# Kernel optimization log

Hardware: AMD Instinct MI355X
Metric: run time of the kernel (lower is better)

## Reference

```python
import jax, jax.numpy as jnp
import numpy as np

N_NODES = 100000
N_EDGES = 1600000
N_GRAPHS = 256
IN_C = 64
HID = 128
OUT = 128
BN_EPS = 1e-5


def setup_inputs() -> dict:
    key = jax.random.key(0)
    ks = jax.random.split(key, 24)
    x = jax.random.normal(ks[0], (N_NODES, IN_C), jnp.float32)
    edge_index = jax.random.randint(ks[1], (2, N_EDGES), 0, N_NODES, dtype=jnp.int64 if jax.config.jax_enable_x64 else jnp.int32)
    batch = jnp.sort(jax.random.randint(ks[2], (N_NODES,), 0, N_GRAPHS))

    def lin(k, i, o):
        return (jax.random.normal(k, (i, o), jnp.float32) / np.float32(np.sqrt(i)))

    d = {"x": x, "edge_index": edge_index, "batch": batch}
    in_dims = [IN_C, HID, HID]
    for l in range(3):
        d[f"w1_{l}"] = lin(ks[3 + 6 * l], in_dims[l], HID)
        d[f"b1_{l}"] = jnp.zeros((HID,), jnp.float32)
        d[f"w2_{l}"] = lin(ks[4 + 6 * l], HID, HID)
        d[f"b2_{l}"] = jnp.zeros((HID,), jnp.float32)
        d[f"gamma_{l}"] = jnp.ones((HID,), jnp.float32)
        d[f"beta_{l}"] = jnp.zeros((HID,), jnp.float32)
    d["proj_w"] = lin(ks[22], HID, OUT)
    d["proj_b"] = jnp.zeros((OUT,), jnp.float32)
    return d


def _gin_forward(x, edge_index, batch, layers, proj_w, proj_b):
    src, dst = edge_index[0], edge_index[1]
    h = x
    for (w1, b1, w2, b2, g, b) in layers:
        # GINConv (eps=0, aggr='add'): MLP(h_i + sum_{j->i} h_j)
        agg = jax.ops.segment_sum(h[src], dst, num_segments=h.shape[0])
        z = h + agg
        z = jax.nn.relu(z @ w1 + b1) @ w2 + b2
        # BatchNorm1d, training mode (biased batch stats)
        mean = z.mean(axis=0)
        var = z.var(axis=0)
        z = (z - mean) * jax.lax.rsqrt(var + BN_EPS) * g + b
        h = jax.nn.relu(z)
    # global_mean_pool over graph ids
    s = jax.ops.segment_sum(h, batch, num_segments=N_GRAPHS)
    cnt = jax.ops.segment_sum(jnp.ones((h.shape[0], 1), h.dtype), batch, num_segments=N_GRAPHS)
    hg = s / jnp.maximum(cnt, 1.0)
    return hg @ proj_w + proj_b


def reference(x, edge_index, batch,
              w1_0, b1_0, w2_0, b2_0, gamma_0, beta_0,
              w1_1, b1_1, w2_1, b2_1, gamma_1, beta_1,
              w1_2, b1_2, w2_2, b2_2, gamma_2, beta_2,
              proj_w, proj_b):
    layers = [
        (w1_0, b1_0, w2_0, b2_0, gamma_0, beta_0),
        (w1_1, b1_1, w2_1, b2_1, gamma_1, beta_1),
        (w1_2, b1_2, w2_2, b2_2, gamma_2, beta_2),
    ]
    return _gin_forward(x, edge_index, batch, layers, proj_w, proj_b)
```

## Files before the change

### kernel.cpp

```cpp
#include <hip/hip_runtime.h>

#define N_NODES 100000
#define N_EDGES 1600000
#define N_GRAPHS 256
#define HID 128
#define BN_EPS 1e-5f

#define NT 1563
#define EB 4096
#define RB 391
#define MB 1563

typedef __bf16 bf16x8 __attribute__((ext_vector_type(8)));
typedef __bf16 bf16x4 __attribute__((ext_vector_type(4)));
typedef __bf16 bf16x2 __attribute__((ext_vector_type(2)));
typedef float f32x4 __attribute__((ext_vector_type(4)));

__global__ __launch_bounds__(256) void prep_all_kernel(
    const float* __restrict__ wa, const float* __restrict__ wb,
    const float* __restrict__ wc, const float* __restrict__ wd,
    const float* __restrict__ we, const float* __restrict__ wf,
    __bf16* __restrict__ wt) {
  int idx = blockIdx.x * 256 + threadIdx.x;
  if (idx >= 90112) return;
  const float* w;
  int K, local;
  if (idx < 8192) { w = wa; K = 64; local = idx; }
  else {
    int s = (idx - 8192) / 16384;
    local = (idx - 8192) - s * 16384;
    K = 128;
    w = (s == 0) ? wb : (s == 1) ? wc : (s == 2) ? wd : (s == 3) ? we : wf;
  }
  int n = local / K, k = local - n * K;
  wt[idx] = (__bf16)w[k * 128 + n];
}

__global__ __launch_bounds__(256) void x_convert_kernel(const float* __restrict__ x,
                                                        __bf16* __restrict__ xb) {
  int idx = blockIdx.x * 256 + threadIdx.x;
  if (idx >= N_NODES * 16) return;
  f32x4 v = ((const f32x4*)x)[idx];
  bf16x4 o = {(__bf16)v[0], (__bf16)v[1], (__bf16)v[2], (__bf16)v[3]};
  ((bf16x4*)xb)[idx] = o;
}

__global__ __launch_bounds__(256) void tile_hist_kernel(const int* __restrict__ ei,
                                                        int* __restrict__ tcnt) {
  __shared__ int hist[NT];
  int t = threadIdx.x;
  for (int i = t; i < NT; i += 256) hist[i] = 0;
  __syncthreads();
  int base = blockIdx.x * EB;
#pragma unroll 4
  for (int i = 0; i < EB / 256; i++) {
    int e = base + i * 256 + t;
    if (e < N_EDGES) atomicAdd(&hist[ei[N_EDGES + e] >> 6], 1);
  }
  __syncthreads();
  for (int i = t; i < NT; i += 256) {
    int h = hist[i];
    if (h) atomicAdd(&tcnt[i], h);
  }
}

__global__ __launch_bounds__(256) void tile_scan_kernel(const int* __restrict__ tcnt,
                                                        int* __restrict__ tstart,
                                                        int* __restrict__ gcursor) {
  __shared__ int ps[256];
  int t = threadIdx.x;
  const int CH = (NT + 255) / 256;
  int lo = t * CH, hi = min(lo + CH, NT);
  int s = 0;
  for (int i = lo; i < hi; i++) s += tcnt[i];
  ps[t] = s;
  __syncthreads();
  for (int off = 1; off < 256; off <<= 1) {
    int v = ps[t];
    int u = (t >= off) ? ps[t - off] : 0;
    __syncthreads();
    ps[t] = v + u;
    __syncthreads();
  }
  int base = (t == 0) ? 0 : ps[t - 1];
  for (int i = lo; i < hi; i++) {
    tstart[i] = base;
    gcursor[i] = base;
    base += tcnt[i];
  }
  if (t == 0) tstart[NT] = N_EDGES;
}

__global__ __launch_bounds__(256) void reorder2_kernel(const int* __restrict__ ei,
                                                       int* __restrict__ gcursor,
                                                       int* __restrict__ epack) {
  __shared__ int hist[NT];
  int t = threadIdx.x;
  for (int i = t; i < NT; i += 256) hist[i] = 0;
  __syncthreads();
  int base = blockIdx.x * EB;
#pragma unroll 4
  for (int i = 0; i < EB / 256; i++) {
    int e = base + i * 256 + t;
    if (e < N_EDGES) atomicAdd(&hist[ei[N_EDGES + e] >> 6], 1);
  }
  __syncthreads();
  for (int i = t; i < NT; i += 256) {
    int h = hist[i];
    if (h) hist[i] = atomicAdd(&gcursor[i], h);
  }
  __syncthreads();
#pragma unroll 4
  for (int i = 0; i < EB / 256; i++) {
    int e = base + i * 256 + t;
    if (e < N_EDGES) {
      int d = ei[N_EDGES + e];
      int s = ei[e];
      int pos = atomicAdd(&hist[d >> 6], 1);
      epack[pos] = (s << 6) | (d & 63);
    }
  }
}

__global__ __launch_bounds__(256) void row_sort_kernel(const int* __restrict__ tstart,
                                                       const int* __restrict__ epack,
                                                       int* __restrict__ starts,
                                                       int* __restrict__ srcs) {
  __shared__ int cnt[64];
  __shared__ int rbase[65];
  __shared__ int rofs[64];
  int t = threadIdx.x, b = blockIdx.x;
  int ts = tstart[b], te = tstart[b + 1];
  if (t < 64) cnt[t] = 0;
  __syncthreads();
  for (int i = ts + t; i < te; i += 256) atomicAdd(&cnt[epack[i] & 63], 1);
  __syncthreads();
  if (t == 0) {
    int a = 0;
    for (int r = 0; r < 64; r++) { rbase[r] = a; a += cnt[r]; }
    rbase[64] = a;
  }
  __syncthreads();
  if (t < 64) rofs[t] = ts + rbase[t];
  if (t <= 64) {
    int gr = b * 64 + t;
    if (gr <= N_NODES) starts[gr] = ts + rbase[t];
  }
  __syncthreads();
  for (int i = ts + t; i < te; i += 256) {
    int p = epack[i];
    int pos = atomicAdd(&rofs[p & 63], 1);
    srcs[pos] = p >> 6;
  }
}

__global__ __launch_bounds__(256) void h_apply_kernel(const __bf16* __restrict__ u,
                                                      const float* __restrict__ bnab,
                                                      __bf16* __restrict__ h) {
  int idx = blockIdx.x * 256 + threadIdx.x;
  if (idx >= N_NODES * (HID / 8)) return;
  int c8 = idx & 15;
  bf16x8 v = ((const bf16x8*)u)[idx];
  f32x4 a0 = ((const f32x4*)bnab)[c8 * 2];
  f32x4 a1 = ((const f32x4*)bnab)[c8 * 2 + 1];
  f32x4 b0 = ((const f32x4*)(bnab + HID))[c8 * 2];
  f32x4 b1 = ((const f32x4*)(bnab + HID))[c8 * 2 + 1];
  bf16x8 o;
#pragma unroll
  for (int k = 0; k < 4; k++) {
    o[k] = (__bf16)fmaxf(fmaf(a0[k], (float)v[k], b0[k]), 0.f);
    o[4 + k] = (__bf16)fmaxf(fmaf(a1[k], (float)v[4 + k], b1[k]), 0.f);
  }
  ((bf16x8*)h)[idx] = o;
}

template <int C>
__global__ __launch_bounds__(256) void gather_kernel(const __bf16* __restrict__ h,
                                                     const int* __restrict__ starts,
                                                     const int* __restrict__ srcs,
                                                     __bf16* __restrict__ z) {
  const int lane = threadIdx.x & 63;
  const int row = blockIdx.x * 4 + (threadIdx.x >> 6);
  if (row >= N_NODES) return;
  int e0 = starts[row], e1 = starts[row + 1];
  int deg = e1 - e0;
  int idxv = srcs[min(e0 + lane, N_EDGES - 1)];
  int dcap = min(deg, 64);
  if constexpr (C == 64) {
    float acc = (float)h[(size_t)row * 64 + lane];
    float s0 = 0.f, s1 = 0.f, s2 = 0.f, s3 = 0.f, s4 = 0.f, s5 = 0.f, s6 = 0.f, s7 = 0.f;
    int j = 0;
    for (; j + 7 < dcap; j += 8) {
      int i0 = __builtin_amdgcn_readlane(idxv, j);
      int i1 = __builtin_amdgcn_readlane(idxv, j + 1);
      int i2 = __builtin_amdgcn_readlane(idxv, j + 2);
      int i3 = __builtin_amdgcn_readlane(idxv, j + 3);
      int i4 = __builtin_amdgcn_readlane(idxv, j + 4);
      int i5 = __builtin_amdgcn_readlane(idxv, j + 5);
      int i6 = __builtin_amdgcn_readlane(idxv, j + 6);
      int i7 = __builtin_amdgcn_readlane(idxv, j + 7);
      float v0 = (float)h[(size_t)i0 * 64 + lane];
      float v1 = (float)h[(size_t)i1 * 64 + lane];
      float v2 = (float)h[(size_t)i2 * 64 + lane];
      float v3 = (float)h[(size_t)i3 * 64 + lane];
      float v4 = (float)h[(size_t)i4 * 64 + lane];
      float v5 = (float)h[(size_t)i5 * 64 + lane];
      float v6 = (float)h[(size_t)i6 * 64 + lane];
      float v7 = (float)h[(size_t)i7 * 64 + lane];
      s0 += v0; s1 += v1; s2 += v2; s3 += v3;
      s4 += v4; s5 += v5; s6 += v6; s7 += v7;
    }
    for (; j < dcap; j++) {
      int i0 = __builtin_amdgcn_readlane(idxv, j);
      s0 += (float)h[(size_t)i0 * 64 + lane];
    }
    for (int e = e0 + 64; e < e1; e++) s0 += (float)h[(size_t)srcs[e] * 64 + lane];
    acc += ((s0 + s1) + (s2 + s3)) + ((s4 + s5) + (s6 + s7));
    z[(size_t)row * 64 + lane] = (__bf16)acc;
  } else {
    bf16x2 sv = *(const bf16x2*)(h + (size_t)row * 128 + lane * 2);
    float ax = (float)sv[0], ay = (float)sv[1];
    float2 s0 = {0.f, 0.f}, s1 = {0.f, 0.f}, s2 = {0.f, 0.f}, s3 = {0.f, 0.f};
    float2 s4 = {0.f, 0.f}, s5 = {0.f, 0.f}, s6 = {0.f, 0.f}, s7 = {0.f, 0.f};
    int j = 0;
    for (; j + 7 < dcap; j += 8) {
      int i0 = __builtin_amdgcn_readlane(idxv, j);
      int i1 = __builtin_amdgcn_readlane(idxv, j + 1);
      int i2 = __builtin_amdgcn_readlane(idxv, j + 2);
      int i3 = __builtin_amdgcn_readlane(idxv, j + 3);
      int i4 = __builtin_amdgcn_readlane(idxv, j + 4);
      int i5 = __builtin_amdgcn_readlane(idxv, j + 5);
      int i6 = __builtin_amdgcn_readlane(idxv, j + 6);
      int i7 = __builtin_amdgcn_readlane(idxv, j + 7);
      bf16x2 v0 = *(const bf16x2*)(h + (size_t)i0 * 128 + lane * 2);
      bf16x2 v1 = *(const bf16x2*)(h + (size_t)i1 * 128 + lane * 2);
      bf16x2 v2 = *(const bf16x2*)(h + (size_t)i2 * 128 + lane * 2);
      bf16x2 v3 = *(const bf16x2*)(h + (size_t)i3 * 128 + lane * 2);
      bf16x2 v4 = *(const bf16x2*)(h + (size_t)i4 * 128 + lane * 2);
      bf16x2 v5 = *(const bf16x2*)(h + (size_t)i5 * 128 + lane * 2);
      bf16x2 v6 = *(const bf16x2*)(h + (size_t)i6 * 128 + lane * 2);
      bf16x2 v7 = *(const bf16x2*)(h + (size_t)i7 * 128 + lane * 2);
      s0.x += (float)v0[0]; s0.y += (float)v0[1];
      s1.x += (float)v1[0]; s1.y += (float)v1[1];
      s2.x += (float)v2[0]; s2.y += (float)v2[1];
      s3.x += (float)v3[0]; s3.y += (float)v3[1];
      s4.x += (float)v4[0]; s4.y += (float)v4[1];
      s5.x += (float)v5[0]; s5.y += (float)v5[1];
      s6.x += (float)v6[0]; s6.y += (float)v6[1];
      s7.x += (float)v7[0]; s7.y += (float)v7[1];
    }
    for (; j < dcap; j++) {
      int i0 = __builtin_amdgcn_readlane(idxv, j);
      bf16x2 vv = *(const bf16x2*)(h + (size_t)i0 * 128 + lane * 2);
      s0.x += (float)vv[0]; s0.y += (float)vv[1];
    }
    for (int e = e0 + 64; e < e1; e++) {
      bf16x2 vv = *(const bf16x2*)(h + (size_t)srcs[e] * 128 + lane * 2);
      s0.x += (float)vv[0]; s0.y += (float)vv[1];
    }
    ax += ((s0.x + s1.x) + (s2.x + s3.x)) + ((s4.x + s5.x) + (s6.x + s7.x));
    ay += ((s0.y + s1.y) + (s2.y + s3.y)) + ((s4.y + s5.y) + (s6.y + s7.y));
    bf16x2 z2 = {(__bf16)ax, (__bf16)ay};
    *(bf16x2*)(z + (size_t)row * 128 + lane * 2) = z2;
  }
}

template <int CIN>
__global__ __launch_bounds__(256) void mlp_kernel(
    const __bf16* __restrict__ z, const __bf16* __restrict__ w1t,
    const float* __restrict__ b1, const __bf16* __restrict__ w2t,
    const float* __restrict__ b2, __bf16* __restrict__ u,
    float* __restrict__ part) {
  constexpr int ZS = CIN + 8;
  constexpr int TS = HID + 8;
  constexpr int US = 132;
  constexpr int ZB = 64 * ZS * 2;
  constexpr int TB = 64 * TS * 2;
  constexpr int UB = 64 * US * 4;
  constexpr int SB = (ZB + TB) > UB ? (ZB + TB) : UB;
  __shared__ __align__(16) char smem[SB];
  __bf16* zt = (__bf16*)smem;
  __bf16* tt = (__bf16*)(smem + ZB);

  const int t = threadIdx.x;
  const int wave = t >> 6;
  const int lane = t & 63;
  const int l16 = lane & 15;
  const int quad = lane >> 4;
  const int rowbase = blockIdx.x * 64;
  const int nvalid = min(64, N_NODES - rowbase);

  {
    constexpr int CH = CIN / 8;
    const bf16x8 zero8 = {};
    for (int f = t; f < 64 * CH; f += 256) {
      int r = f / CH, c = f - r * CH;
      int gr = rowbase + r;
      bf16x8 v = (gr < N_NODES) ? *(const bf16x8*)(z + (size_t)gr * CIN + c * 8) : zero8;
      *(bf16x8*)(zt + r * ZS + c * 8) = v;
    }
  }
  __syncthreads();

  const f32x4 zero4 = {0.f, 0.f, 0.f, 0.f};
  f32x4 acc[8];

  {
#pragma unroll
    for (int ct = 0; ct < 8; ct++) acc[ct] = zero4;
    const __bf16* arow = zt + (wave * 16 + l16) * ZS + quad * 8;
#pragma unroll
    for (int ks = 0; ks < CIN / 32; ks++) {
      bf16x8 af = *(const bf16x8*)(arow + ks * 32);
#pragma unroll
      for (int ct = 0; ct < 8; ct++) {
        bf16x8 bfr = *(const bf16x8*)(w1t + (ct * 16 + l16) * CIN + ks * 32 + quad * 8);
        acc[ct] = __builtin_amdgcn_mfma_f32_16x16x32_bf16(af, bfr, acc[ct], 0, 0, 0);
      }
    }
#pragma unroll
    for (int ct = 0; ct < 8; ct++) {
      int col = ct * 16 + l16;
      float bias = b1[col];
#pragma unroll
      for (int r = 0; r < 4; r++) {
        float v = acc[ct][r] + bias;
        tt[(wave * 16 + quad * 4 + r) * TS + col] = (__bf16)(v > 0.f ? v : 0.f);
      }
    }
  }
  __syncthreads();

  {
#pragma unroll
    for (int ct = 0; ct < 8; ct++) acc[ct] = zero4;
    const __bf16* arow = tt + (wave * 16 + l16) * TS + quad * 8;
#pragma unroll
    for (int ks = 0; ks < HID / 32; ks++) {
      bf16x8 af = *(const bf16x8*)(arow + ks * 32);
#pragma unroll
      for (int ct = 0; ct < 8; ct++) {
        bf16x8 bfr = *(const bf16x8*)(w2t + (ct * 16 + l16) * HID + ks * 32 + quad * 8);
        acc[ct] = __builtin_amdgcn_mfma_f32_16x16x32_bf16(af, bfr, acc[ct], 0, 0, 0);
      }
    }
  }
  __syncthreads();
  float* uo = (float*)smem;
#pragma unroll
  for (int ct = 0; ct < 8; ct++) {
    int col = ct * 16 + l16;
    float bias = b2[col];
#pragma unroll
    for (int r = 0; r < 4; r++) {
      uo[(wave * 16 + quad * 4 + r) * US + col] = acc[ct][r] + bias;
    }
  }
  __syncthreads();

  for (int f = t; f < 64 * 32; f += 256) {
    int r = f >> 5, c4 = f & 31;
    if (r < nvalid) {
      f32x4 v = *(const f32x4*)(uo + r * US + c4 * 4);
      bf16x4 o = {(__bf16)v[0], (__bf16)v[1], (__bf16)v[2], (__bf16)v[3]};
      *(bf16x4*)(u + (size_t)(rowbase + r) * HID + c4 * 4) = o;
    }
  }
  if (t < HID) {
    float s = 0.f, sq = 0.f;
    for (int r = 0; r < nvalid; r++) {
      float v = uo[r * US + t];
      s += v;
      sq += v * v;
    }
    part[(size_t)blockIdx.x * 256 + t] = s;
    part[(size_t)blockIdx.x * 256 + HID + t] = sq;
  }
}

__global__ __launch_bounds__(256) void bn_stats_kernel(const float* __restrict__ part,
                                                       const float* __restrict__ gamma,
                                                       const float* __restrict__ beta,
                                                       float* __restrict__ bnab) {
  __shared__ float ss[256], qq[256];
  int c = blockIdx.x;
  int t = threadIdx.x;
  float s = 0.f, q = 0.f;
  for (int b = t; b < MB; b += 256) {
    s += part[(size_t)b * 256 + c];
    q += part[(size_t)b * 256 + HID + c];
  }
  ss[t] = s; qq[t] = q;
  __syncthreads();
  for (int off = 128; off > 0; off >>= 1) {
    if (t < off) { ss[t] += ss[t + off]; qq[t] += qq[t + off]; }
    __syncthreads();
  }
  if (t == 0) {
    const float invN = 1.f / (float)N_NODES;
    float mean = ss[0] * invN;
    float var = qq[0] * invN - mean * mean;
    float a = gamma[c] * rsqrtf(var + BN_EPS);
    bnab[c] = a;
    bnab[HID + c] = beta[c] - mean * a;
  }
}

__global__ __launch_bounds__(128) void bn_apply_pool_kernel(const __bf16* __restrict__ u,
                                                            const float* __restrict__ bnab,
                                                            const int* __restrict__ batch,
                                                            float* __restrict__ pool) {
  int c = threadIdx.x;
  int r0 = blockIdx.x * 64;
  if (r0 >= N_NODES) return;
  int rend = min(r0 + 64, N_NODES);
  float a = bnab[c], b = bnab[HID + c];
  float accv = 0.f;
  int curg = -1;
  for (int r = r0; r < rend; r++) {
    int g = batch[r];
    if (g != curg) {
      if (curg >= 0) atomicAdd(&pool[curg * HID + c], accv);
      curg = g;
      accv = 0.f;
    }
    float v = (float)u[(size_t)r * HID + c];
    v = v * a + b;
    accv += (v > 0.f ? v : 0.f);
  }
  if (curg >= 0) atomicAdd(&pool[curg * HID + c], accv);
}

__global__ __launch_bounds__(256) void count_kernel(const int* __restrict__ batch,
                                                    int* __restrict__ counts) {
  int t = blockIdx.x * 256 + threadIdx.x;
  int r0 = t * 64;
  if (r0 >= N_NODES) return;
  int rend = min(r0 + 64, N_NODES);
  int curg = batch[r0], cnt = 0;
  for (int r = r0; r < rend; r++) {
    int g = batch[r];
    if (g != curg) {
      atomicAdd(&counts[curg], cnt);
      curg = g;
      cnt = 1;
    } else {
      cnt++;
    }
  }
  atomicAdd(&counts[curg], cnt);
}

__global__ __launch_bounds__(128) void pool_proj_kernel(const float* __restrict__ pool,
                                                        const int* __restrict__ counts,
                                                        const float* __restrict__ pw,
                                                        const float* __restrict__ pb,
                                                        float* __restrict__ out) {
  int g = blockIdx.x;
  int c = threadIdx.x;
  __shared__ float hg[HID];
  float cnt = (float)max(counts[g], 1);
  hg[c] = pool[g * HID + c] / cnt;
  __syncthreads();
  float acc = pb[c];
#pragma unroll 8
  for (int k = 0; k < HID; k++) acc += hg[k] * pw[k * HID + c];
  out[g * HID + c] = acc;
}

extern "C" void kernel_launch(void* const* d_in, const int* in_sizes, int n_in,
                              void* d_out, int out_size, void* d_ws, size_t ws_size,
                              hipStream_t stream) {
  (void)in_sizes; (void)n_in; (void)out_size; (void)ws_size;
  const float* x = (const float*)d_in[0];
  const int* ei = (const int*)d_in[1];
  const int* batch = (const int*)d_in[2];
  const float* w1[3] = {(const float*)d_in[3], (const float*)d_in[9], (const float*)d_in[15]};
  const float* b1[3] = {(const float*)d_in[4], (const float*)d_in[10], (const float*)d_in[16]};
  const float* w2[3] = {(const float*)d_in[5], (const float*)d_in[11], (const float*)d_in[17]};
  const float* b2[3] = {(const float*)d_in[6], (const float*)d_in[12], (const float*)d_in[18]};
  const float* gm[3] = {(const float*)d_in[7], (const float*)d_in[13], (const float*)d_in[19]};
  const float* bt[3] = {(const float*)d_in[8], (const float*)d_in[14], (const float*)d_in[20]};
  const float* pw = (const float*)d_in[21];
  const float* pb = (const float*)d_in[22];
  float* out = (float*)d_out;

  char* ws = (char*)d_ws;
  __bf16* bufA = (__bf16*)ws;        ws += (size_t)N_NODES * HID * 2;
  __bf16* bufB = (__bf16*)ws;        ws += (size_t)N_NODES * HID * 2;
  __bf16* bufC = (__bf16*)ws;        ws += (size_t)N_NODES * HID * 2;
  __bf16* z0 = (__bf16*)ws;          ws += (size_t)N_NODES * 64 * 2;
  __bf16* xb = (__bf16*)ws;          ws += (size_t)N_NODES * 64 * 2;
  int* srcs = (int*)ws;              ws += (size_t)N_EDGES * 4;
  int* epack = (int*)ws;             ws += (size_t)N_EDGES * 4;
  int* starts = (int*)ws;            ws += (size_t)(N_NODES + 1) * 4;
  int* tcnt = (int*)ws;              ws += NT * 4;
  int* tstart = (int*)ws;            ws += (NT + 1) * 4;
  int* gcursor = (int*)ws;           ws += NT * 4;
  ws = (char*)(((uintptr_t)ws + 63) & ~(uintptr_t)63);
  float* part = (float*)ws;          ws += (size_t)MB * 256 * 4;
  __bf16* wt_all = (__bf16*)ws;      ws += 90112 * 2;
  ws = (char*)(((uintptr_t)ws + 63) & ~(uintptr_t)63);
  float* bnab = (float*)ws;          ws += 256 * 4;
  float* pool = (float*)ws;          ws += N_GRAPHS * HID * 4;
  int* counts = (int*)ws;            ws += N_GRAPHS * 4;

  __bf16* w1t0 = wt_all;
  __bf16* w2t0 = wt_all + 8192;
  __bf16* w1t1 = wt_all + 24576;
  __bf16* w2t1 = wt_all + 40960;
  __bf16* w1t2 = wt_all + 57344;
  __bf16* w2t2 = wt_all + 73728;

  const int mlp_blocks = MB;
  const int gat_blocks = (N_NODES + 3) / 4;
  const int app_blocks = (N_NODES * (HID / 8) + 255) / 256;

  prep_all_kernel<<<(90112 + 255) / 256, 256, 0, stream>>>(
      w1[0], w2[0], w1[1], w2[1], w1[2], w2[2], wt_all);
  x_convert_kernel<<<(N_NODES * 16 + 255) / 256, 256, 0, stream>>>(x, xb);

  hipMemsetAsync(tcnt, 0, NT * 4, stream);
  tile_hist_kernel<<<RB, 256, 0, stream>>>(ei, tcnt);
  tile_scan_kernel<<<1, 256, 0, stream>>>(tcnt, tstart, gcursor);
  reorder2_kernel<<<RB, 256, 0, stream>>>(ei, gcursor, epack);
  row_sort_kernel<<<NT, 256, 0, stream>>>(tstart, epack, starts, srcs);

  hipMemsetAsync(pool, 0, (size_t)N_GRAPHS * HID * 4 + N_GRAPHS * 4, stream);
  count_kernel<<<((N_NODES + 63) / 64 + 255) / 256, 256, 0, stream>>>(batch, counts);

  gather_kernel<64><<<gat_blocks, 256, 0, stream>>>(xb, starts, srcs, z0);
  mlp_kernel<64><<<mlp_blocks, 256, 0, stream>>>(z0, w1t0, b1[0], w2t0, b2[0], bufA, part);
  bn_stats_kernel<<<HID, 256, 0, stream>>>(part, gm[0], bt[0], bnab);

  h_apply_kernel<<<app_blocks, 256, 0, stream>>>(bufA, bnab, bufB);
  gather_kernel<128><<<gat_blocks, 256, 0, stream>>>(bufB, starts, srcs, bufC);
  mlp_kernel<128><<<mlp_blocks, 256, 0, stream>>>(bufC, w1t1, b1[1], w2t1, b2[1], bufC, part);
  bn_stats_kernel<<<HID, 256, 0, stream>>>(part, gm[1], bt[1], bnab);

  h_apply_kernel<<<app_blocks, 256, 0, stream>>>(bufC, bnab, bufA);
  gather_kernel<128><<<gat_blocks, 256, 0, stream>>>(bufA, starts, srcs, bufB);
  mlp_kernel<128><<<mlp_blocks, 256, 0, stream>>>(bufB, w1t2, b1[2], w2t2, b2[2], bufB, part);
  bn_stats_kernel<<<HID, 256, 0, stream>>>(part, gm[2], bt[2], bnab);

  bn_apply_pool_kernel<<<mlp_blocks, 128, 0, stream>>>(bufB, bnab, batch, pool);

  pool_proj_kernel<<<N_GRAPHS, 128, 0, stream>>>(pool, counts, pw, pb, out);
}
```

Measured before the change: 611.4 us.

## Fuse neighbor gather into MLP kernel, writing aggregated rows straight to LDS

Result: slower. 693.8 us (+13.5%).

```diff
diff --git a/kernel.cpp b/kernel.cpp
--- a/kernel.cpp
+++ b/kernel.cpp
@@ -174,103 +174,13 @@
   ((bf16x8*)h)[idx] = o;
 }
 
-template <int C>
-__global__ __launch_bounds__(256) void gather_kernel(const __bf16* __restrict__ h,
-                                                     const int* __restrict__ starts,
-                                                     const int* __restrict__ srcs,
-                                                     __bf16* __restrict__ z) {
-  const int lane = threadIdx.x & 63;
-  const int row = blockIdx.x * 4 + (threadIdx.x >> 6);
-  if (row >= N_NODES) return;
-  int e0 = starts[row], e1 = starts[row + 1];
-  int deg = e1 - e0;
-  int idxv = srcs[min(e0 + lane, N_EDGES - 1)];
-  int dcap = min(deg, 64);
-  if constexpr (C == 64) {
-    float acc = (float)h[(size_t)row * 64 + lane];
-    float s0 = 0.f, s1 = 0.f, s2 = 0.f, s3 = 0.f, s4 = 0.f, s5 = 0.f, s6 = 0.f, s7 = 0.f;
-    int j = 0;
-    for (; j + 7 < dcap; j += 8) {
-      int i0 = __builtin_amdgcn_readlane(idxv, j);
-      int i1 = __builtin_amdgcn_readlane(idxv, j + 1);
-      int i2 = __builtin_amdgcn_readlane(idxv, j + 2);
-      int i3 = __builtin_amdgcn_readlane(idxv, j + 3);
-      int i4 = __builtin_amdgcn_readlane(idxv, j + 4);
-      int i5 = __builtin_amdgcn_readlane(idxv, j + 5);
-      int i6 = __builtin_amdgcn_readlane(idxv, j + 6);
-      int i7 = __builtin_amdgcn_readlane(idxv, j + 7);
-      float v0 = (float)h[(size_t)i0 * 64 + lane];
-      float v1 = (float)h[(size_t)i1 * 64 + lane];
-      float v2 = (float)h[(size_t)i2 * 64 + lane];
-      float v3 = (float)h[(size_t)i3 * 64 + lane];
-      float v4 = (float)h[(size_t)i4 * 64 + lane];
-      float v5 = (float)h[(size_t)i5 * 64 + lane];
-      float v6 = (float)h[(size_t)i6 * 64 + lane];
-      float v7 = (float)h[(size_t)i7 * 64 + lane];
-      s0 += v0; s1 += v1; s2 += v2; s3 += v3;
-      s4 += v4; s5 += v5; s6 += v6; s7 += v7;
-    }
-    for (; j < dcap; j++) {
-      int i0 = __builtin_amdgcn_readlane(idxv, j);
-      s0 += (float)h[(size_t)i0 * 64 + lane];
-    }
-    for (int e = e0 + 64; e < e1; e++) s0 += (float)h[(size_t)srcs[e] * 64 + lane];
-    acc += ((s0 + s1) + (s2 + s3)) + ((s4 + s5) + (s6 + s7));
-    z[(size_t)row * 64 + lane] = (__bf16)acc;
-  } else {
-    bf16x2 sv = *(const bf16x2*)(h + (size_t)row * 128 + lane * 2);
-    float ax = (float)sv[0], ay = (float)sv[1];
-    float2 s0 = {0.f, 0.f}, s1 = {0.f, 0.f}, s2 = {0.f, 0.f}, s3 = {0.f, 0.f};
-    float2 s4 = {0.f, 0.f}, s5 = {0.f, 0.f}, s6 = {0.f, 0.f}, s7 = {0.f, 0.f};
-    int j = 0;
-    for (; j + 7 < dcap; j += 8) {
-      int i0 = __builtin_amdgcn_readlane(idxv, j);
-      int i1 = __builtin_amdgcn_readlane(idxv, j + 1);
-      int i2 = __builtin_amdgcn_readlane(idxv, j + 2);
-      int i3 = __builtin_amdgcn_readlane(idxv, j + 3);
-      int i4 = __builtin_amdgcn_readlane(idxv, j + 4);
-      int i5 = __builtin_amdgcn_readlane(idxv, j + 5);
-      int i6 = __builtin_amdgcn_readlane(idxv, j + 6);
-      int i7 = __builtin_amdgcn_readlane(idxv, j + 7);
-      bf16x2 v0 = *(const bf16x2*)(h + (size_t)i0 * 128 + lane * 2);
-      bf16x2 v1 = *(const bf16x2*)(h + (size_t)i1 * 128 + lane * 2);
-      bf16x2 v2 = *(const bf16x2*)(h + (size_t)i2 * 128 + lane * 2);
-      bf16x2 v3 = *(const bf16x2*)(h + (size_t)i3 * 128 + lane * 2);
-      bf16x2 v4 = *(const bf16x2*)(h + (size_t)i4 * 128 + lane * 2);
-      bf16x2 v5 = *(const bf16x2*)(h + (size_t)i5 * 128 + lane * 2);
-      bf16x2 v6 = *(const bf16x2*)(h + (size_t)i6 * 128 + lane * 2);
-      bf16x2 v7 = *(const bf16x2*)(h + (size_t)i7 * 128 + lane * 2);
-      s0.x += (float)v0[0]; s0.y += (float)v0[1];
-      s1.x += (float)v1[0]; s1.y += (float)v1[1];
-      s2.x += (float)v2[0]; s2.y += (float)v2[1];
-      s3.x += (float)v3[0]; s3.y += (float)v3[1];
-      s4.x += (float)v4[0]; s4.y += (float)v4[1];
-      s5.x += (float)v5[0]; s5.y += (float)v5[1];
-      s6.x += (float)v6[0]; s6.y += (float)v6[1];
-      s7.x += (float)v7[0]; s7.y += (float)v7[1];
-    }
-    for (; j < dcap; j++) {
-      int i0 = __builtin_amdgcn_readlane(idxv, j);
-      bf16x2 vv = *(const bf16x2*)(h + (size_t)i0 * 128 + lane * 2);
-      s0.x += (float)vv[0]; s0.y += (float)vv[1];
-    }
-    for (int e = e0 + 64; e < e1; e++) {
-      bf16x2 vv = *(const bf16x2*)(h + (size_t)srcs[e] * 128 + lane * 2);
-      s0.x += (float)vv[0]; s0.y += (float)vv[1];
-    }
-    ax += ((s0.x + s1.x) + (s2.x + s3.x)) + ((s4.x + s5.x) + (s6.x + s7.x));
-    ay += ((s0.y + s1.y) + (s2.y + s3.y)) + ((s4.y + s5.y) + (s6.y + s7.y));
-    bf16x2 z2 = {(__bf16)ax, (__bf16)ay};
-    *(bf16x2*)(z + (size_t)row * 128 + lane * 2) = z2;
-  }
-}
-
 template <int CIN>
-__global__ __launch_bounds__(256) void mlp_kernel(
-    const __bf16* __restrict__ z, const __bf16* __restrict__ w1t,
-    const float* __restrict__ b1, const __bf16* __restrict__ w2t,
-    const float* __restrict__ b2, __bf16* __restrict__ u,
-    float* __restrict__ part) {
+__global__ __launch_bounds__(256) void gmlp_kernel(
+    const __bf16* __restrict__ h, const int* __restrict__ starts,
+    const int* __restrict__ srcs,
+    const __bf16* __restrict__ w1t, const float* __restrict__ b1,
+    const __bf16* __restrict__ w2t, const float* __restrict__ b2,
+    __bf16* __restrict__ u, float* __restrict__ part) {
   constexpr int ZS = CIN + 8;
   constexpr int TS = HID + 8;
   constexpr int US = 132;
@@ -290,14 +200,99 @@
   const int rowbase = blockIdx.x * 64;
   const int nvalid = min(64, N_NODES - rowbase);
 
-  {
-    constexpr int CH = CIN / 8;
-    const bf16x8 zero8 = {};
-    for (int f = t; f < 64 * CH; f += 256) {
-      int r = f / CH, c = f - r * CH;
-      int gr = rowbase + r;
-      bf16x8 v = (gr < N_NODES) ? *(const bf16x8*)(z + (size_t)gr * CIN + c * 8) : zero8;
-      *(bf16x8*)(zt + r * ZS + c * 8) = v;
+#pragma unroll 1
+  for (int i = 0; i < 16; ++i) {
+    const int rl = wave * 16 + i;
+    const int row = rowbase + rl;
+    if (row >= N_NODES) {
+      if constexpr (CIN == 64) {
+        zt[rl * ZS + lane] = (__bf16)0.f;
+      } else {
+        bf16x2 zz = {(__bf16)0.f, (__bf16)0.f};
+        *(bf16x2*)(zt + rl * ZS + lane * 2) = zz;
+      }
+      continue;
+    }
+    int e0 = starts[row], e1 = starts[row + 1];
+    int deg = e1 - e0;
+    int idxv = srcs[min(e0 + lane, N_EDGES - 1)];
+    int dcap = min(deg, 64);
+    if constexpr (CIN == 64) {
+      float acc = (float)h[(size_t)row * 64 + lane];
+      float s0 = 0.f, s1 = 0.f, s2 = 0.f, s3 = 0.f, s4 = 0.f, s5 = 0.f, s6 = 0.f, s7 = 0.f;
+      int j = 0;
+      for (; j + 7 < dcap; j += 8) {
+        int i0 = __builtin_amdgcn_readlane(idxv, j);
+        int i1 = __builtin_amdgcn_readlane(idxv, j + 1);
+        int i2 = __builtin_amdgcn_readlane(idxv, j + 2);
+        int i3 = __builtin_amdgcn_readlane(idxv, j + 3);
+        int i4 = __builtin_amdgcn_readlane(idxv, j + 4);
+        int i5 = __builtin_amdgcn_readlane(idxv, j + 5);
+        int i6 = __builtin_amdgcn_readlane(idxv, j + 6);
+        int i7 = __builtin_amdgcn_readlane(idxv, j + 7);
+        float v0 = (float)h[(size_t)i0 * 64 + lane];
+        float v1 = (float)h[(size_t)i1 * 64 + lane];
+        float v2 = (float)h[(size_t)i2 * 64 + lane];
+        float v3 = (float)h[(size_t)i3 * 64 + lane];
+        float v4 = (float)h[(size_t)i4 * 64 + lane];
+        float v5 = (float)h[(size_t)i5 * 64 + lane];
+        float v6 = (float)h[(size_t)i6 * 64 + lane];
+        float v7 = (float)h[(size_t)i7 * 64 + lane];
+        s0 += v0; s1 += v1; s2 += v2; s3 += v3;
+        s4 += v4; s5 += v5; s6 += v6; s7 += v7;
+      }
+      for (; j < dcap; j++) {
+        int i0 = __builtin_amdgcn_readlane(idxv, j);
+        s0 += (float)h[(size_t)i0 * 64 + lane];
+      }
+      for (int e = e0 + 64; e < e1; e++) s0 += (float)h[(size_t)srcs[e] * 64 + lane];
+      acc += ((s0 + s1) + (s2 + s3)) + ((s4 + s5) + (s6 + s7));
+      zt[rl * ZS + lane] = (__bf16)acc;
+    } else {
+      bf16x2 sv = *(const bf16x2*)(h + (size_t)row * 128 + lane * 2);
+      float ax = (float)sv[0], ay = (float)sv[1];
+      float2 s0 = {0.f, 0.f}, s1 = {0.f, 0.f}, s2 = {0.f, 0.f}, s3 = {0.f, 0.f};
+      float2 s4 = {0.f, 0.f}, s5 = {0.f, 0.f}, s6 = {0.f, 0.f}, s7 = {0.f, 0.f};
+      int j = 0;
+      for (; j + 7 < dcap; j += 8) {
+        int i0 = __builtin_amdgcn_readlane(idxv, j);
+        int i1 = __builtin_amdgcn_readlane(idxv, j + 1);
+        int i2 = __builtin_amdgcn_readlane(idxv, j + 2);
+        int i3 = __builtin_amdgcn_readlane(idxv, j + 3);
+        int i4 = __builtin_amdgcn_readlane(idxv, j + 4);
+        int i5 = __builtin_amdgcn_readlane(idxv, j + 5);
+        int i6 = __builtin_amdgcn_readlane(idxv, j + 6);
+        int i7 = __builtin_amdgcn_readlane(idxv, j + 7);
+        bf16x2 v0 = *(const bf16x2*)(h + (size_t)i0 * 128 + lane * 2);
+        bf16x2 v1 = *(const bf16x2*)(h + (size_t)i1 * 128 + lane * 2);
+        bf16x2 v2 = *(const bf16x2*)(h + (size_t)i2 * 128 + lane * 2);
+        bf16x2 v3 = *(const bf16x2*)(h + (size_t)i3 * 128 + lane * 2);
+        bf16x2 v4 = *(const bf16x2*)(h + (size_t)i4 * 128 + lane * 2);
+        bf16x2 v5 = *(const bf16x2*)(h + (size_t)i5 * 128 + lane * 2);
+        bf16x2 v6 = *(const bf16x2*)(h + (size_t)i6 * 128 + lane * 2);
+        bf16x2 v7 = *(const bf16x2*)(h + (size_t)i7 * 128 + lane * 2);
+        s0.x += (float)v0[0]; s0.y += (float)v0[1];
+        s1.x += (float)v1[0]; s1.y += (float)v1[1];
+        s2.x += (float)v2[0]; s2.y += (float)v2[1];
+        s3.x += (float)v3[0]; s3.y += (float)v3[1];
+        s4.x += (float)v4[0]; s4.y += (float)v4[1];
+        s5.x += (float)v5[0]; s5.y += (float)v5[1];
+        s6.x += (float)v6[0]; s6.y += (float)v6[1];
+        s7.x += (float)v7[0]; s7.y += (float)v7[1];
+      }
+      for (; j < dcap; j++) {
+        int i0 = __builtin_amdgcn_readlane(idxv, j);
+        bf16x2 vv = *(const bf16x2*)(h + (size_t)i0 * 128 + lane * 2);
+        s0.x += (float)vv[0]; s0.y += (float)vv[1];
+      }
+      for (int e = e0 + 64; e < e1; e++) {
+        bf16x2 vv = *(const bf16x2*)(h + (size_t)srcs[e] * 128 + lane * 2);
+        s0.x += (float)vv[0]; s0.y += (float)vv[1];
+      }
+      ax += ((s0.x + s1.x) + (s2.x + s3.x)) + ((s4.x + s5.x) + (s6.x + s7.x));
+      ay += ((s0.y + s1.y) + (s2.y + s3.y)) + ((s4.y + s5.y) + (s6.y + s7.y));
+      bf16x2 z2 = {(__bf16)ax, (__bf16)ay};
+      *(bf16x2*)(zt + rl * ZS + lane * 2) = z2;
     }
   }
   __syncthreads();
@@ -504,6 +499,7 @@
   float* bnab = (float*)ws;          ws += 256 * 4;
   float* pool = (float*)ws;          ws += N_GRAPHS * HID * 4;
   int* counts = (int*)ws;            ws += N_GRAPHS * 4;
+  (void)z0;
 
   __bf16* w1t0 = wt_all;
   __bf16* w2t0 = wt_all + 8192;
@@ -512,8 +508,6 @@
   __bf16* w1t2 = wt_all + 57344;
   __bf16* w2t2 = wt_all + 73728;
 
-  const int mlp_blocks = MB;
-  const int gat_blocks = (N_NODES + 3) / 4;
   const int app_blocks = (N_NODES * (HID / 8) + 255) / 256;
 
   prep_all_kernel<<<(90112 + 255) / 256, 256, 0, stream>>>(
@@ -529,21 +523,18 @@
   hipMemsetAsync(pool, 0, (size_t)N_GRAPHS * HID * 4 + N_GRAPHS * 4, stream);
   count_kernel<<<((N_NODES + 63) / 64 + 255) / 256, 256, 0, stream>>>(batch, counts);
 
-  gather_kernel<64><<<gat_blocks, 256, 0, stream>>>(xb, starts, srcs, z0);
-  mlp_kernel<64><<<mlp_blocks, 256, 0, stream>>>(z0, w1t0, b1[0], w2t0, b2[0], bufA, part);
+  gmlp_kernel<64><<<MB, 256, 0, stream>>>(xb, starts, srcs, w1t0, b1[0], w2t0, b2[0], bufA, part);
   bn_stats_kernel<<<HID, 256, 0, stream>>>(part, gm[0], bt[0], bnab);
 
   h_apply_kernel<<<app_blocks, 256, 0, stream>>>(bufA, bnab, bufB);
-  gather_kernel<128><<<gat_blocks, 256, 0, stream>>>(bufB, starts, srcs, bufC);
-  mlp_kernel<128><<<mlp_blocks, 256, 0, stream>>>(bufC, w1t1, b1[1], w2t1, b2[1], bufC, part);
+  gmlp_kernel<128><<<MB, 256, 0, stream>>>(bufB, starts, srcs, w1t1, b1[1], w2t1, b2[1], bufC, part);
   bn_stats_kernel<<<HID, 256, 0, stream>>>(part, gm[1], bt[1], bnab);
 
   h_apply_kernel<<<app_blocks, 256, 0, stream>>>(bufC, bnab, bufA);
-  gather_kernel<128><<<gat_blocks, 256, 0, stream>>>(bufA, starts, srcs, bufB);
-  mlp_kernel<128><<<mlp_blocks, 256, 0, stream>>>(bufB, w1t2, b1[2], w2t2, b2[2], bufB, part);
+  gmlp_kernel<128><<<MB, 256, 0, stream>>>(bufA, starts, srcs, w1t2, b1[2], w2t2, b2[2], bufB, part);
   bn_stats_kernel<<<HID, 256, 0, stream>>>(part, gm[2], bt[2], bnab);
 
-  bn_apply_pool_kernel<<<mlp_blocks, 128, 0, stream>>>(bufB, bnab, batch, pool);
+  bn_apply_pool_kernel<<<MB, 128, 0, stream>>>(bufB, bnab, batch, pool);
 
   pool_proj_kernel<<<N_GRAPHS, 128, 0, stream>>>(pool, counts, pw, pb, out);
 }
```
